# Kernel tuning notes

Hardware: AMD Instinct MI355X
Metric: run time of the kernel (lower is better)

The kernel has to match this reference:

```python
import jax, jax.numpy as jnp
import numpy as np
from jax import lax

WIN_SIZE = 11
WIN_SIGMA = 1.5
ALPHA = 0.84
K1, K2 = 0.01, 0.03
DATA_RANGE = 1.0


def _gaussian_window(size, sigma):
    coords = jnp.arange(size, dtype=jnp.float32) - (size - 1) / 2.0
    g = jnp.exp(-(coords ** 2) / (2.0 * sigma ** 2))
    return g / jnp.sum(g)


def _gaussian_filter(x, win):
    # separable depthwise gaussian blur, VALID padding (pytorch_msssim style)
    C = x.shape[1]
    kH = jnp.tile(win.reshape(1, 1, -1, 1), (C, 1, 1, 1))  # OIHW, depthwise
    kW = jnp.tile(win.reshape(1, 1, 1, -1), (C, 1, 1, 1))
    x = lax.conv_general_dilated(x, kH, (1, 1), 'VALID', feature_group_count=C)
    x = lax.conv_general_dilated(x, kW, (1, 1), 'VALID', feature_group_count=C)
    return x


def _ssim(X, Y, win):
    C1 = (K1 * DATA_RANGE) ** 2
    C2 = (K2 * DATA_RANGE) ** 2
    mu1 = _gaussian_filter(X, win)
    mu2 = _gaussian_filter(Y, win)
    mu1_sq = mu1 * mu1
    mu2_sq = mu2 * mu2
    mu1_mu2 = mu1 * mu2
    sigma1_sq = _gaussian_filter(X * X, win) - mu1_sq
    sigma2_sq = _gaussian_filter(Y * Y, win) - mu2_sq
    sigma12 = _gaussian_filter(X * Y, win) - mu1_mu2
    cs_map = (2.0 * sigma12 + C2) / (sigma1_sq + sigma2_sq + C2)
    ssim_map = ((2.0 * mu1_mu2 + C1) / (mu1_sq + mu2_sq + C1)) * cs_map
    return jnp.mean(ssim_map)


def setup_inputs() -> dict:
    key = jax.random.key(0)
    k1, k2 = jax.random.split(key)
    shape = (16, 3, 512, 512)
    pred = jax.random.uniform(k1, shape, dtype=jnp.float32)
    target = jax.random.uniform(k2, shape, dtype=jnp.float32)
    return {"pred": pred, "target": target}


def reference(pred, target):
    pred = jnp.clip(pred, 0.0, 1.0)
    target = jnp.clip(target, 0.0, 1.0)
    mse_loss = jnp.mean((pred - target) ** 2)
    win = _gaussian_window(WIN_SIZE, WIN_SIGMA)
    ssim_loss = 1.0 - _ssim(pred, target, win)
    return (1.0 - ALPHA) * mse_loss + ALPHA * ssim_loss
```

## Files before the change

kernel.cpp:

```cpp
#include <hip/hip_runtime.h>
#include <hip/hip_fp16.h>


#define OH 8

struct __align__(8) H2x2 { __half2 a, b; };

__global__ __launch_bounds__(256, 4) void ssim_fused(
    const float* __restrict__ pred, const float* __restrict__ targ,
    float2* __restrict__ part)
{
    __shared__ __half2 sPh2[5 * 4 * 512];

    const float wv[11] = {
        0.00102838f, 0.00759876f, 0.03600078f, 0.10936070f, 0.21300554f,
        0.26601173f,
        0.21300554f, 0.10936070f, 0.03600078f, 0.00759876f, 0.00102838f };
    __half2 wh[11];
    #pragma unroll
    for (int k = 0; k < 11; ++k) wh[k] = __float2half2_rn(wv[k]);

    const int tid = threadIdx.x;
    const int bid = ((int)blockIdx.x & 7) * 384 + ((int)blockIdx.x >> 3);
    const int img = bid >> 6;
    const int oy0 = (bid & 63) * OH;
    const float* __restrict__ P = pred + (size_t)img * (512 * 512);
    const float* __restrict__ T = targ + (size_t)img * (512 * 512);

    const int c0 = tid * 2;

    __half2 va[5][OH];
    #pragma unroll
    for (int p = 0; p < 5; ++p)
        #pragma unroll
        for (int j = 0; j < OH; ++j) va[p][j] = __float2half2_rn(0.0f);

    float mse_acc = 0.f;

    #pragma unroll
    for (int i = 0; i < OH + 10; ++i) {
        int gy = oy0 + i; if (gy > 511) gy = 511;
        const float2 xv = *reinterpret_cast<const float2*>(P + gy * 512 + c0);
        const float2 yv = *reinterpret_cast<const float2*>(T + gy * 512 + c0);
        const float x0 = __builtin_amdgcn_fmed3f(xv.x, 0.f, 1.f);
        const float x1 = __builtin_amdgcn_fmed3f(xv.y, 0.f, 1.f);
        const float y0 = __builtin_amdgcn_fmed3f(yv.x, 0.f, 1.f);
        const float y1 = __builtin_amdgcn_fmed3f(yv.y, 0.f, 1.f);
        if (i < OH) {
            const float d0 = x0 - y0, d1 = x1 - y1;
            mse_acc = fmaf(d0, d0, mse_acc);
            mse_acc = fmaf(d1, d1, mse_acc);
        }
        const __half2 hx = __float22half2_rn(make_float2(x0, x1));
        const __half2 hy = __float22half2_rn(make_float2(y0, y1));
        const __half2 pr[5] = { hx, hy, __hmul2(hx, hx), __hmul2(hy, hy),
                                __hmul2(hx, hy) };
        #pragma unroll
        for (int j = 0; j < OH; ++j) {
            const int k = i - j;
            if (k >= 0 && k <= 10) {
                #pragma unroll
                for (int p = 0; p < 5; ++p)
                    va[p][j] = __hfma2(wh[k], pr[p], va[p][j]);
            }
        }
    }

    #pragma unroll
    for (int p = 0; p < 5; ++p)
        #pragma unroll
        for (int jp = 0; jp < 4; ++jp) {
            const __half2 a = va[p][2 * jp], b = va[p][2 * jp + 1];
            H2x2 st;
            st.a = __halves2half2(__low2half(a),  __low2half(b));
            st.b = __halves2half2(__high2half(a), __high2half(b));
            *reinterpret_cast<H2x2*>(&sPh2[(p * 4 + jp) * 512 + c0]) = st;
        }

    __syncthreads();

    const int rp   = tid >> 6;
    const int lane = tid & 63;
    const int oc0  = lane * 8;
    const int rc0 = (oc0 > 496) ? 492 : oc0;
    const int t2  = (rc0 + 16 > 510) ? 510 : (rc0 + 16);

    __half2 hc[5][8];
    union U4 { float4 f4; __half2 h2[4]; };
    union U2 { float2 f2; __half2 h2[2]; };
    #pragma unroll
    for (int p = 0; p < 5; ++p) {
        const __half2* rowb = &sPh2[(p * 4 + rp) * 512];
        __half2 win[18];
        U4 u0, u1, u2, u3; U2 u4;
        u0.f4 = *reinterpret_cast<const float4*>(rowb + rc0);
        u1.f4 = *reinterpret_cast<const float4*>(rowb + rc0 + 4);
        u2.f4 = *reinterpret_cast<const float4*>(rowb + rc0 + 8);
        u3.f4 = *reinterpret_cast<const float4*>(rowb + rc0 + 12);
        u4.f2 = *reinterpret_cast<const float2*>(rowb + t2);
        #pragma unroll
        for (int q = 0; q < 4; ++q) {
            win[q]      = u0.h2[q];
            win[q + 4]  = u1.h2[q];
            win[q + 8]  = u2.h2[q];
            win[q + 12] = u3.h2[q];
        }
        win[16] = u4.h2[0]; win[17] = u4.h2[1];
        #pragma unroll
        for (int cc = 0; cc < 8; ++cc) {
            __half2 s = __float2half2_rn(0.0f);
            #pragma unroll
            for (int t = 0; t < 11; ++t)
                s = __hfma2(wh[t], win[cc + t], s);
            hc[p][cc] = s;
        }
    }

    float ssim_acc = 0.f;
    {
        const float C1 = 0.0001f, C2 = 0.0009f;
        const int ylo = oy0 + 2 * rp;
        const bool vlo = ylo < 502, vhi = (ylo + 1) < 502;
        #pragma unroll
        for (int cc = 0; cc < 8; ++cc) {
            if (oc0 + cc < 502) {
                #pragma unroll
                for (int h = 0; h < 2; ++h) {
                    if (h ? vhi : vlo) {
                        const float mu1 = h ? __high2float(hc[0][cc]) : __low2float(hc[0][cc]);
                        const float mu2 = h ? __high2float(hc[1][cc]) : __low2float(hc[1][cc]);
                        const float exx = h ? __high2float(hc[2][cc]) : __low2float(hc[2][cc]);
                        const float eyy = h ? __high2float(hc[3][cc]) : __low2float(hc[3][cc]);
                        const float exy = h ? __high2float(hc[4][cc]) : __low2float(hc[4][cc]);
                        const float m11 = mu1 * mu1, m22 = mu2 * mu2, m12 = mu1 * mu2;
                        const float s1  = exx - m11;
                        const float s2  = eyy - m22;
                        const float s12 = exy - m12;
                        const float num = (2.f * m12 + C1) * (2.f * s12 + C2);
                        const float den = (m11 + m22 + C1) * (s1 + s2 + C2);
                        ssim_acc += num * __builtin_amdgcn_rcpf(den);
                    }
                }
            }
        }
    }

    float vx = mse_acc, vy = ssim_acc;
    #pragma unroll
    for (int off = 32; off > 0; off >>= 1) {
        vx += __shfl_down(vx, off);
        vy += __shfl_down(vy, off);
    }
    __syncthreads();
    float* redf = reinterpret_cast<float*>(sPh2);
    const int wave = tid >> 6;
    if ((tid & 63) == 0) { redf[wave * 2] = vx; redf[wave * 2 + 1] = vy; }
    __syncthreads();
    if (tid == 0) {
        part[bid] = make_float2(redf[0] + redf[2] + redf[4] + redf[6],
                                redf[1] + redf[3] + redf[5] + redf[7]);
    }
}

__global__ __launch_bounds__(256) void ssim_reduce(
    const float2* __restrict__ part, float* __restrict__ out)
{
    __shared__ float red[8];
    const int tid = threadIdx.x;
    const float4* p4 = reinterpret_cast<const float4*>(part);
    float ms = 0.f, ss = 0.f;
    #pragma unroll
    for (int k = 0; k < 6; ++k) {
        const float4 v = p4[tid + k * 256];
        ms += v.x + v.z; ss += v.y + v.w;
    }
    #pragma unroll
    for (int off = 32; off > 0; off >>= 1) {
        ms += __shfl_down(ms, off);
        ss += __shfl_down(ss, off);
    }
    const int wave = tid >> 6;
    if ((tid & 63) == 0) { red[wave * 2] = ms; red[wave * 2 + 1] = ss; }
    __syncthreads();
    if (tid == 0) {
        const float msum = red[0] + red[2] + red[4] + red[6];
        const float ssum = red[1] + red[3] + red[5] + red[7];
        const float mse  = msum * (1.0f / 12582912.0f);
        const float ssim = ssum * (1.0f / 12096192.0f);
        out[0] = 0.16f * mse + 0.84f * (1.0f - ssim);
    }
}

extern "C" void kernel_launch(void* const* d_in, const int* in_sizes, int n_in,
                              void* d_out, int out_size, void* d_ws, size_t ws_size,
                              hipStream_t stream)
{
    const float* pred = (const float*)d_in[0];
    const float* targ = (const float*)d_in[1];
    float2* part = (float2*)d_ws;

    ssim_fused<<<3072, 256, 0, stream>>>(pred, targ, part);
    ssim_reduce<<<1, 256, 0, stream>>>(part, (float*)d_out);
}
```

Baseline: 43.50 us.

## Halve shared-memory staging and process horizontal pass in two halves for occupancy

The shared buffer for vertically blurred rows is cut in half by running the horizontal pass twice, each time over two packed row-pairs. Each thread now computes 4 output columns instead of 8, which shrinks the window and accumulator registers, and the launch-bounds occupancy hint rises from 4 to 5 blocks. The aim is more resident blocks per CU through lower LDS and register use. The cost is an extra barrier round and more redundant window loads from shared memory, since overlap between neighbouring threads grows.

Measured after the change: 66.02 us. 51.8% more time.

```diff
diff --git a/kernel.cpp b/kernel.cpp
--- a/kernel.cpp
+++ b/kernel.cpp
@@ -6,11 +6,11 @@
 
 struct __align__(8) H2x2 { __half2 a, b; };
 
-__global__ __launch_bounds__(256, 4) void ssim_fused(
+__global__ __launch_bounds__(256, 5) void ssim_fused(
     const float* __restrict__ pred, const float* __restrict__ targ,
     float2* __restrict__ part)
 {
-    __shared__ __half2 sPh2[5 * 4 * 512];
+    __shared__ __half2 sPh2[5 * 2 * 512 + 8];
 
     const float wv[11] = {
         0.00102838f, 0.00759876f, 0.03600078f, 0.10936070f, 0.21300554f,
@@ -66,63 +66,65 @@
         }
     }
 
-    #pragma unroll
-    for (int p = 0; p < 5; ++p)
-        #pragma unroll
-        for (int jp = 0; jp < 4; ++jp) {
-            const __half2 a = va[p][2 * jp], b = va[p][2 * jp + 1];
-            H2x2 st;
-            st.a = __halves2half2(__low2half(a),  __low2half(b));
-            st.b = __halves2half2(__high2half(a), __high2half(b));
-            *reinterpret_cast<H2x2*>(&sPh2[(p * 4 + jp) * 512 + c0]) = st;
-        }
-
-    __syncthreads();
-
-    const int rp   = tid >> 6;
-    const int lane = tid & 63;
-    const int oc0  = lane * 8;
-    const int rc0 = (oc0 > 496) ? 492 : oc0;
-    const int t2  = (rc0 + 16 > 510) ? 510 : (rc0 + 16);
-
-    __half2 hc[5][8];
-    union U4 { float4 f4; __half2 h2[4]; };
-    union U2 { float2 f2; __half2 h2[2]; };
-    #pragma unroll
-    for (int p = 0; p < 5; ++p) {
-        const __half2* rowb = &sPh2[(p * 4 + rp) * 512];
-        __half2 win[18];
-        U4 u0, u1, u2, u3; U2 u4;
-        u0.f4 = *reinterpret_cast<const float4*>(rowb + rc0);
-        u1.f4 = *reinterpret_cast<const float4*>(rowb + rc0 + 4);
-        u2.f4 = *reinterpret_cast<const float4*>(rowb + rc0 + 8);
-        u3.f4 = *reinterpret_cast<const float4*>(rowb + rc0 + 12);
-        u4.f2 = *reinterpret_cast<const float2*>(rowb + t2);
-        #pragma unroll
-        for (int q = 0; q < 4; ++q) {
-            win[q]      = u0.h2[q];
-            win[q + 4]  = u1.h2[q];
-            win[q + 8]  = u2.h2[q];
-            win[q + 12] = u3.h2[q];
-        }
-        win[16] = u4.h2[0]; win[17] = u4.h2[1];
-        #pragma unroll
-        for (int cc = 0; cc < 8; ++cc) {
-            __half2 s = __float2half2_rn(0.0f);
+    float ssim_acc = 0.f;
+    const float C1 = 0.0001f, C2 = 0.0009f;
+
+    const int rpl = tid >> 7;
+    const int oc0 = (tid & 127) * 4;
+    const int rc0 = (oc0 >= 504) ? 496 : oc0;
+
+    #pragma unroll
+    for (int half = 0; half < 2; ++half) {
+        if (half) __syncthreads();
+
+        #pragma unroll
+        for (int p = 0; p < 5; ++p)
             #pragma unroll
-            for (int t = 0; t < 11; ++t)
-                s = __hfma2(wh[t], win[cc + t], s);
-            hc[p][cc] = s;
-        }
-    }
-
-    float ssim_acc = 0.f;
-    {
-        const float C1 = 0.0001f, C2 = 0.0009f;
+            for (int jpl = 0; jpl < 2; ++jpl) {
+                const int jp = 2 * half + jpl;
+                const __half2 a = va[p][2 * jp], b = va[p][2 * jp + 1];
+                H2x2 st;
+                st.a = __halves2half2(__low2half(a),  __low2half(b));
+                st.b = __halves2half2(__high2half(a), __high2half(b));
+                *reinterpret_cast<H2x2*>(&sPh2[(p * 2 + jpl) * 512 + c0]) = st;
+            }
+
+        __syncthreads();
+
+        __half2 hc[5][4];
+        union U4 { float4 f4; __half2 h2[4]; };
+        union U2 { float2 f2; __half2 h2[2]; };
+        #pragma unroll
+        for (int p = 0; p < 5; ++p) {
+            const __half2* base = &sPh2[(p * 2 + rpl) * 512 + rc0];
+            __half2 win[14];
+            U4 u0, u1, u2; U2 u3;
+            u0.f4 = *reinterpret_cast<const float4*>(base);
+            u1.f4 = *reinterpret_cast<const float4*>(base + 4);
+            u2.f4 = *reinterpret_cast<const float4*>(base + 8);
+            u3.f2 = *reinterpret_cast<const float2*>(base + 12);
+            #pragma unroll
+            for (int q = 0; q < 4; ++q) {
+                win[q]     = u0.h2[q];
+                win[q + 4] = u1.h2[q];
+                win[q + 8] = u2.h2[q];
+            }
+            win[12] = u3.h2[0]; win[13] = u3.h2[1];
+            #pragma unroll
+            for (int cc = 0; cc < 4; ++cc) {
+                __half2 s = __float2half2_rn(0.0f);
+                #pragma unroll
+                for (int t = 0; t < 11; ++t)
+                    s = __hfma2(wh[t], win[cc + t], s);
+                hc[p][cc] = s;
+            }
+        }
+
+        const int rp  = 2 * half + rpl;
         const int ylo = oy0 + 2 * rp;
         const bool vlo = ylo < 502, vhi = (ylo + 1) < 502;
         #pragma unroll
-        for (int cc = 0; cc < 8; ++cc) {
+        for (int cc = 0; cc < 4; ++cc) {
             if (oc0 + cc < 502) {
                 #pragma unroll
                 for (int h = 0; h < 2; ++h) {
```
